# Optimization experiments

Measured on AMD Instinct MI355X. Metric: run time of the kernel, lower is better.

Reference implementation:

```python
import jax, jax.numpy as jnp
import numpy as np

D_MODEL = 1024
N_HEADS = 16
D_HEAD = D_MODEL // N_HEADS
D_FF = 4096
MAX_ITERS = 2
B, T = 8, 1024
LN_EPS = 1e-5


def _layernorm(x, g, b):
    m = jnp.mean(x, axis=-1, keepdims=True)
    v = jnp.mean(jnp.square(x - m), axis=-1, keepdims=True)
    return (x - m) * jax.lax.rsqrt(v + LN_EPS) * g + b


def setup_inputs() -> dict:
    key = jax.random.key(0)
    ks = jax.random.split(key, 16)
    s = 0.02
    inp = {
        "z": jax.random.normal(ks[0], (B, T, D_MODEL), dtype=jnp.float32),
        # per-head Q/K/V projections stacked over heads: [H, D, Dh], bias [H, Dh]
        "Wq": jax.random.normal(ks[1], (N_HEADS, D_MODEL, D_HEAD), dtype=jnp.float32) * s,
        "bq": jnp.zeros((N_HEADS, D_HEAD), dtype=jnp.float32),
        "Wk": jax.random.normal(ks[2], (N_HEADS, D_MODEL, D_HEAD), dtype=jnp.float32) * s,
        "bk": jnp.zeros((N_HEADS, D_HEAD), dtype=jnp.float32),
        "Wv": jax.random.normal(ks[3], (N_HEADS, D_MODEL, D_HEAD), dtype=jnp.float32) * s,
        "bv": jnp.zeros((N_HEADS, D_HEAD), dtype=jnp.float32),
        "Wo": jax.random.normal(ks[4], (D_MODEL, D_MODEL), dtype=jnp.float32) * s,
        "bo": jnp.zeros((D_MODEL,), dtype=jnp.float32),
        "W1": jax.random.normal(ks[5], (D_MODEL, D_FF), dtype=jnp.float32) * s,
        "b1": jnp.zeros((D_FF,), dtype=jnp.float32),
        "W2": jax.random.normal(ks[6], (D_FF, D_MODEL), dtype=jnp.float32) * s,
        "b2": jnp.zeros((D_MODEL,), dtype=jnp.float32),
        "g1": jnp.ones((D_MODEL,), dtype=jnp.float32),
        "be1": jnp.zeros((D_MODEL,), dtype=jnp.float32),
        "g2": jnp.ones((D_MODEL,), dtype=jnp.float32),
        "be2": jnp.zeros((D_MODEL,), dtype=jnp.float32),
    }
    return inp


def reference(z, Wq, bq, Wk, bk, Wv, bv, Wo, bo, W1, b1, W2, b2, g1, be1, g2, be2):
    # Controller outputs (alphas/state/aux) are unused by the original forward -> omitted.
    # Dropout is inference-identity.
    scale = 1.0 / jnp.sqrt(jnp.asarray(D_HEAD, dtype=z.dtype))
    z_refined = z
    for _ in range(MAX_ITERS):
        # batched per-head projections: [B,H,T,Dh]
        q = jnp.einsum('btd,hdk->bhtk', z, Wq) + bq[None, :, None, :]
        k = jnp.einsum('btd,hdk->bhtk', z, Wk) + bk[None, :, None, :]
        v = jnp.einsum('btd,hdk->bhtk', z, Wv) + bv[None, :, None, :]
        scores = jnp.einsum('bhtk,bhsk->bhts', q, k) * scale  # [B,H,T,T]
        attn = jax.nn.softmax(scores, axis=-1)
        o = jnp.einsum('bhts,bhsk->bhtk', attn, v)  # [B,H,T,Dh]
        # concat heads in order (matches torch.cat over head list)
        o = jnp.transpose(o, (0, 2, 1, 3)).reshape(z.shape[0], z.shape[1], D_MODEL)
        attn_out = o @ Wo + bo
        z = _layernorm(z + attn_out, g1, be1)
        z_refined = z
        ffn = jnp.maximum(z @ W1 + b1, 0.0) @ W2 + b2
        z = _layernorm(z + ffn, g2, be2)
    return z_refined
```

## Files before the change

### kernel.cpp

```cpp
#include <hip/hip_runtime.h>
#include <hip/hip_bf16.h>

typedef __bf16 bf16t;
typedef bf16t bf16x4 __attribute__((ext_vector_type(4)));
typedef bf16t bf16x8 __attribute__((ext_vector_type(8)));
typedef float f32x4 __attribute__((ext_vector_type(4)));

#define BT 8192
#define TT 1024
#define DM 1024
#define DFF 4096

static __device__ __forceinline__ f32x4 mfma16(bf16x8 a, bf16x8 b, f32x4 c) {
  return __builtin_amdgcn_mfma_f32_16x16x32_bf16(a, b, c, 0, 0, 0);
}
static __device__ __forceinline__ bf16x8 ld8(const bf16t* p0, const bf16t* p1) {
  bf16x4 lo = *(const bf16x4*)p0;
  bf16x4 hi = *(const bf16x4*)p1;
  return __builtin_shufflevector(lo, hi, 0, 1, 2, 3, 4, 5, 6, 7);
}
static __device__ __forceinline__ f32x4 f4zero() {
  f32x4 z = {0.f, 0.f, 0.f, 0.f};
  return z;
}
static __device__ __forceinline__ f32x4 vmax4(f32x4 a, f32x4 b) {
  f32x4 r;
#pragma unroll
  for (int i = 0; i < 4; i++) r[i] = fmaxf(a[i], b[i]);
  return r;
}
static __device__ __forceinline__ void gld16(const bf16t* g, bf16t* l) {
  __builtin_amdgcn_global_load_lds((const __attribute__((address_space(1))) void*)g,
                                   (__attribute__((address_space(3))) void*)l, 16, 0, 0);
}

__global__ __launch_bounds__(256) void cvt_kernel(const float* __restrict__ in,
                                                  bf16t* __restrict__ out, long n) {
  long i = ((long)blockIdx.x * 256 + threadIdx.x) * 4;
  if (i >= n) return;
  f32x4 v = *(const f32x4*)&in[i];
  bf16x4 o = {(bf16t)v[0], (bf16t)v[1], (bf16t)v[2], (bf16t)v[3]};
  *(bf16x4*)&out[i] = o;
}

__global__ __launch_bounds__(256) void tcvt_kernel(const float* __restrict__ in,
                                                   bf16t* __restrict__ out, int M, int N) {
  __shared__ float T[64][65];
  const int t = threadIdx.x;
  const int ty = t >> 6, tx = t & 63;
  const long n0 = (long)blockIdx.x * 64, m0 = (long)blockIdx.y * 64;
#pragma unroll
  for (int p = 0; p < 16; ++p) {
    int a = ty * 16 + p;
    T[a][tx] = in[(m0 + a) * N + n0 + tx];
  }
  __syncthreads();
#pragma unroll
  for (int p = 0; p < 16; ++p) {
    int r = ty * 16 + p;
    out[(n0 + r) * M + m0 + tx] = (bf16t)T[tx][r];
  }
}

__global__ __launch_bounds__(256) void vtrans_kernel(const bf16t* __restrict__ qkv,
                                                     bf16t* __restrict__ vT) {
  __shared__ bf16t T[64][72];
  const int bh = blockIdx.x;
  const int b = bh >> 4, h = bh & 15;
  const int tt = blockIdx.y;
  const int t = threadIdx.x;
  const int ty = t >> 6, tx = t & 63;
  const long srcbase = ((long)b * TT + tt * 64) * 3072 + 2048 + h * 64;
#pragma unroll
  for (int p = 0; p < 16; ++p) {
    int a = ty * 16 + p;
    T[a][tx] = qkv[srcbase + (long)a * 3072 + tx];
  }
  __syncthreads();
  const long dstbase = ((long)bh * 64) * 1024 + tt * 64;
#pragma unroll
  for (int p = 0; p < 16; ++p) {
    int d = ty * 16 + p;
    vT[dstbase + (long)d * 1024 + tx] = T[tx][d];
  }
}

__global__ __launch_bounds__(256) void pack_qkv_t_kernel(const float* __restrict__ Wq,
                                                         const float* __restrict__ Wk,
                                                         const float* __restrict__ Wv,
                                                         bf16t* __restrict__ WT) {
  __shared__ float T[64][65];
  const int bx = blockIdx.x;
  const int sel = bx >> 4, h = bx & 15;
  const float* src = ((sel == 0) ? Wq : (sel == 1) ? Wk : Wv) + (long)h * 65536;
  const long nbase = (long)sel * 1024 + h * 64;
  const long m0 = (long)blockIdx.y * 64;
  const int t = threadIdx.x;
  const int ty = t >> 6, tx = t & 63;
#pragma unroll
  for (int p = 0; p < 16; ++p) {
    int a = ty * 16 + p;
    T[a][tx] = src[(m0 + a) * 64 + tx];
  }
  __syncthreads();
#pragma unroll
  for (int p = 0; p < 16; ++p) {
    int r = ty * 16 + p;
    WT[(nbase + r) * 1024 + m0 + tx] = (bf16t)T[tx][r];
  }
}

__global__ __launch_bounds__(256) void pack_bias_kernel(const float* __restrict__ bq,
                                                        const float* __restrict__ bk,
                                                        const float* __restrict__ bv,
                                                        float* __restrict__ bqkv) {
  int i = blockIdx.x * 256 + threadIdx.x;
  if (i >= 3072) return;
  int sel = i >> 10, c = i & 1023;
  bqkv[i] = ((sel == 0) ? bq : (sel == 1) ? bk : bv)[c];
}

template <int EPI>
__global__ __launch_bounds__(256) void gemm_kernel(
    const bf16t* __restrict__ A, const bf16t* __restrict__ Bt,
    const float* __restrict__ bias, const float* __restrict__ resid,
    void* __restrict__ Cout, int M, int N, int K) {
  __shared__ bf16t As[3 * 128 * 32];
  __shared__ bf16t Bs[3 * 128 * 32];
  const int tid = threadIdx.x;
  const int lane = tid & 63;
  const int wid = tid >> 6;
  const int wr = wid >> 1, wc = wid & 1;
  const int g = lane >> 4, lr = lane & 15;

  const int gy = M >> 7;
  const int nwg = gridDim.x;
  const int chunk = nwg >> 3;
  const int wg = blockIdx.x;
  const int lid = (wg & 7) * chunk + (wg >> 3);
  const int gsz = gy << 3;
  const int group = lid / gsz;
  const int rem = lid - group * gsz;
  const int rr = rem >> 3;
  const int cc = (group << 3) + (rem & 7);
  const long brow = (long)rr * 128;
  const long bcol = (long)cc * 128;

  f32x4 acc[4][4];
#pragma unroll
  for (int i = 0; i < 4; i++)
#pragma unroll
    for (int j = 0; j < 4; j++) acc[i][j] = f4zero();

  const int srow = tid >> 2;
  const int csrc = (tid & 3) ^ ((tid >> 3) & 3);
  const bf16t* gA = &A[(brow + srow) * (long)K + 8 * csrc];
  const bf16t* gB = &Bt[(bcol + srow) * (long)K + 8 * csrc];
  bf16t* lA = As + wid * 512;
  bf16t* lB = Bs + wid * 512;

  const int xsw = ((lr >> 1) & 3) << 3;
  const int ra0 = (4 * g) ^ xsw;
  const int ra1 = (16 + 4 * g) ^ xsw;

  auto stage = [&](int buf, int k0) {
    gld16(gA + k0, lA + buf * 4096);
    gld16(gA + k0 + (long)64 * K, lA + buf * 4096 + 2048);
    gld16(gB + k0, lB + buf * 4096);
    gld16(gB + k0 + (long)64 * K, lB + buf * 4096 + 2048);
  };

  const int nt = K >> 5;
  stage(0, 0);
  stage(1, 32);
  asm volatile("s_waitcnt vmcnt(4)" ::: "memory");
  __builtin_amdgcn_s_barrier();
  __builtin_amdgcn_sched_barrier(0);

  for (int t = 0; t < nt; ++t) {
    const int k2 = (t + 2) << 5;
    const bool pf = (k2 < K);
    if (pf) stage((t + 2) % 3, k2);

    const bf16t* bufA = As + (t % 3) * 4096;
    const bf16t* bufB = Bs + (t % 3) * 4096;
    bf16x8 af[4], bfv[4];
#pragma unroll
    for (int i = 0; i < 4; i++) {
      const bf16t* r = bufA + (wr * 64 + i * 16 + lr) * 32;
      af[i] = ld8(r + ra0, r + ra1);
    }
#pragma unroll
    for (int j = 0; j < 4; j++) {
      const bf16t* c = bufB + (wc * 64 + j * 16 + lr) * 32;
      bfv[j] = ld8(c + ra0, c + ra1);
    }
#pragma unroll
    for (int i = 0; i < 4; i++)
#pragma unroll
      for (int j = 0; j < 4; j++) acc[i][j] = mfma16(af[i], bfv[j], acc[i][j]);

    if (t + 1 < nt) {
      if (pf)
        asm volatile("s_waitcnt vmcnt(4)" ::: "memory");
      else
        asm volatile("s_waitcnt vmcnt(0)" ::: "memory");
      __builtin_amdgcn_s_barrier();
      __builtin_amdgcn_sched_barrier(0);
    }
  }

#pragma unroll
  for (int j = 0; j < 4; j++) {
    int col = (int)bcol + wc * 64 + j * 16 + lr;
    float bval = bias ? bias[col] : 0.f;
#pragma unroll
    for (int i = 0; i < 4; i++) {
      long row0 = brow + wr * 64 + i * 16 + 4 * g;
#pragma unroll
      for (int r2 = 0; r2 < 4; r2++) {
        long row = row0 + r2;
        float v = acc[i][j][r2] + bval;
        if (EPI == 0) {
          ((bf16t*)Cout)[row * N + col] = (bf16t)v;
        } else if (EPI == 1) {
          ((bf16t*)Cout)[row * N + col] = (bf16t)fmaxf(v, 0.f);
        } else {
          ((float*)Cout)[row * N + col] = v + resid[row * N + col];
        }
      }
    }
  }
}

__global__ __launch_bounds__(256) void attn_kernel(const bf16t* __restrict__ qkv,
                                                   const bf16t* __restrict__ vT,
                                                   bf16t* __restrict__ o) {
  const int bh = blockIdx.x;
  const int b = bh >> 4, h = bh & 15;
  const int qt = blockIdx.y;
  const int tid = threadIdx.x;
  const int lane = tid & 63;
  const int w = tid >> 6;
  const int g = lane >> 4, lr = lane & 15;

  __shared__ bf16t Qs[64 * 64];
  __shared__ bf16t Ks[2][64 * 64];
  __shared__ bf16t Vs[2][64 * 64];

  const long rowbase = (long)b * TT;
  const long qrow0 = rowbase + (long)qt * 64;

  const int srow_in_call = w * 8 + (lane >> 3);
  const int schunk = (lane & 7) ^ ((lane >> 3) & 7);
  const int soff = 8 * schunk;

  const bf16t* qsrc = &qkv[(qrow0 + srow_in_call) * 3072 + h * 64 + soff];
  const bf16t* ksrc = &qkv[(rowbase + srow_in_call) * 3072 + 1024 + h * 64 + soff];
  const bf16t* vsrc = &vT[((long)bh * 64 + srow_in_call) * 1024 + soff];
  bf16t* ldst = (bf16t*)((w * 8) * 64);

  auto stageQ = [&]() {
    gld16(qsrc, Qs + (size_t)ldst);
    gld16(qsrc + (long)32 * 3072, Qs + (size_t)ldst + 32 * 64);
  };
  auto stageK = [&](int buf, int kt) {
    const bf16t* s = ksrc + (long)kt * 64 * 3072;
    gld16(s, Ks[buf] + (size_t)ldst);
    gld16(s + (long)32 * 3072, Ks[buf] + (size_t)ldst + 32 * 64);
  };
  auto stageV = [&](int buf, int kt) {
    const bf16t* s = vsrc + kt * 64;
    gld16(s, Vs[buf] + (size_t)ldst);
    gld16(s + (long)32 * 1024, Vs[buf] + (size_t)ldst + 32 * 64);
  };

  stageQ();
  stageK(0, 0);
  stageV(0, 0);
  __syncthreads();

  const int swk = (lr & 7) << 3;
  const int o0 = (4 * g) ^ swk, o1 = (16 + 4 * g) ^ swk;
  const int o2 = (32 + 4 * g) ^ swk, o3 = (48 + 4 * g) ^ swk;

  const bf16t* qrow = Qs + (w * 16 + lr) * 64;
  const bf16x8 qb_lo = ld8(qrow + o0, qrow + o1);
  const bf16x8 qb_hi = ld8(qrow + o2, qrow + o3);

  f32x4 acc_o[4];
#pragma unroll
  for (int j = 0; j < 4; j++) acc_o[j] = f4zero();
  float mrun = -1e30f, lrun = 0.f;

  int cur = 0;
  for (int kt = 0; kt < 16; ++kt) {
    if (kt < 15) {
      stageK(cur ^ 1, kt + 1);
      stageV(cur ^ 1, kt + 1);
    }

    f32x4 s[4];
#pragma unroll
    for (int jt = 0; jt < 4; jt++) {
      const bf16t* krow = Ks[cur] + (jt * 16 + lr) * 64;
      bf16x8 ka_lo = ld8(krow + o0, krow + o1);
      bf16x8 ka_hi = ld8(krow + o2, krow + o3);
      f32x4 t = f4zero();
      t = mfma16(ka_lo, qb_lo, t);
      t = mfma16(ka_hi, qb_hi, t);
      s[jt] = t;
    }

#pragma unroll
    for (int jt = 0; jt < 4; jt++)
#pragma unroll
      for (int r = 0; r < 4; r++) s[jt][r] *= 0.125f;

    f32x4 mv = vmax4(vmax4(s[0], s[1]), vmax4(s[2], s[3]));
    float tm = fmaxf(fmaxf(mv[0], mv[1]), fmaxf(mv[2], mv[3]));
    tm = fmaxf(tm, __shfl_xor(tm, 16, 64));
    tm = fmaxf(tm, __shfl_xor(tm, 32, 64));

    float mnew = fmaxf(mrun, tm);
    float corr = __expf(mrun - mnew);
    mrun = mnew;

    f32x4 sv = f4zero();
#pragma unroll
    for (int jt = 0; jt < 4; jt++)
#pragma unroll
      for (int r = 0; r < 4; r++) {
        float pv = __expf(s[jt][r] - mnew);
        s[jt][r] = pv;
        sv[r] += pv;
      }
    float tsum = sv[0] + sv[1] + sv[2] + sv[3];
    tsum += __shfl_xor(tsum, 16, 64);
    tsum += __shfl_xor(tsum, 32, 64);
    lrun = lrun * corr + tsum;

#pragma unroll
    for (int r = 0; r < 4; r++) {
      float cq = __shfl(corr, 20 * g + r, 64);
#pragma unroll
      for (int dt = 0; dt < 4; dt++) acc_o[dt][r] *= cq;
    }

    bf16x8 pa0, pa1;
#pragma unroll
    for (int r = 0; r < 4; r++) {
      pa0[r] = (bf16t)s[0][r];
      pa0[r + 4] = (bf16t)s[1][r];
      pa1[r] = (bf16t)s[2][r];
      pa1[r + 4] = (bf16t)s[3][r];
    }

#pragma unroll
    for (int dt = 0; dt < 4; dt++) {
      const bf16t* vrow = Vs[cur] + (dt * 16 + lr) * 64;
      bf16x8 vb_lo = ld8(vrow + o0, vrow + o1);
      bf16x8 vb_hi = ld8(vrow + o2, vrow + o3);
      acc_o[dt] = mfma16(pa0, vb_lo, acc_o[dt]);
      acc_o[dt] = mfma16(pa1, vb_hi, acc_o[dt]);
    }

    __syncthreads();
    cur ^= 1;
  }

  float inv = 1.0f / lrun;
#pragma unroll
  for (int r = 0; r < 4; r++) {
    float iq = __shfl(inv, 20 * g + r, 64);
    long row = qrow0 + w * 16 + 4 * g + r;
#pragma unroll
    for (int dt = 0; dt < 4; dt++) {
      o[row * (long)DM + h * 64 + dt * 16 + lr] = (bf16t)(acc_o[dt][r] * iq);
    }
  }
}

__global__ __launch_bounds__(256) void ln_kernel(const float* __restrict__ x,
                                                 const float* __restrict__ gamma,
                                                 const float* __restrict__ beta,
                                                 bf16t* __restrict__ out_bf,
                                                 float* __restrict__ out_f32) {
  const long row = blockIdx.x;
  const int tid = threadIdx.x;
  const float* xr = x + row * DM;
  f32x4 v = *(const f32x4*)&xr[tid * 4];
  float s = v[0] + v[1] + v[2] + v[3];
  float ss = v[0] * v[0] + v[1] * v[1] + v[2] * v[2] + v[3] * v[3];
#pragma unroll
  for (int m = 1; m < 64; m <<= 1) {
    s += __shfl_xor(s, m, 64);
    ss += __shfl_xor(ss, m, 64);
  }
  __shared__ float red[8];
  const int w = tid >> 6, lane = tid & 63;
  if (lane == 0) {
    red[w] = s;
    red[4 + w] = ss;
  }
  __syncthreads();
  s = red[0] + red[1] + red[2] + red[3];
  ss = red[4] + red[5] + red[6] + red[7];
  float mean = s * (1.f / DM);
  float var = ss * (1.f / DM) - mean * mean;
  float inv = rsqrtf(var + 1e-5f);
  f32x4 ga = *(const f32x4*)&gamma[tid * 4];
  f32x4 be = *(const f32x4*)&beta[tid * 4];
  bf16x4 ob;
  f32x4 of;
#pragma unroll
  for (int c = 0; c < 4; c++) {
    float y = (v[c] - mean) * inv * ga[c] + be[c];
    ob[c] = (bf16t)y;
    of[c] = y;
  }
  long base = row * DM + tid * 4;
  if (out_bf) *(bf16x4*)&out_bf[base] = ob;
  if (out_f32) *(f32x4*)&out_f32[base] = of;
}

extern "C" void kernel_launch(void* const* d_in, const int* in_sizes, int n_in,
                              void* d_out, int out_size, void* d_ws, size_t ws_size,
                              hipStream_t stream) {
  const float* z = (const float*)d_in[0];
  const float* Wq = (const float*)d_in[1];
  const float* bq = (const float*)d_in[2];
  const float* Wk = (const float*)d_in[3];
  const float* bk = (const float*)d_in[4];
  const float* Wv = (const float*)d_in[5];
  const float* bv = (const float*)d_in[6];
  const float* Wo = (const float*)d_in[7];
  const float* bo = (const float*)d_in[8];
  const float* W1 = (const float*)d_in[9];
  const float* b1 = (const float*)d_in[10];
  const float* W2 = (const float*)d_in[11];
  const float* b2 = (const float*)d_in[12];
  const float* g1 = (const float*)d_in[13];
  const float* be1 = (const float*)d_in[14];
  const float* g2 = (const float*)d_in[15];
  const float* be2 = (const float*)d_in[16];

  char* p = (char*)d_ws;
  auto alloc = [&](size_t bytes) {
    char* r = p;
    p += (bytes + 255) & ~(size_t)255;
    return r;
  };
  bf16t* wqkvT = (bf16t*)alloc((size_t)3072 * 1024 * 2);
  float* bqkv = (float*)alloc((size_t)3072 * 4);
  bf16t* woT = (bf16t*)alloc((size_t)1024 * 1024 * 2);
  bf16t* w1T = (bf16t*)alloc((size_t)4096 * 1024 * 2);
  bf16t* w2T = (bf16t*)alloc((size_t)1024 * 4096 * 2);
  bf16t* act = (bf16t*)alloc((size_t)BT * 1024 * 2);
  bf16t* obuf = (bf16t*)alloc((size_t)BT * 1024 * 2);
  bf16t* big = (bf16t*)alloc((size_t)BT * 4096 * 2);
  float* tbuf = (float*)alloc((size_t)BT * 1024 * 4);
  float* residf = (float*)alloc((size_t)BT * 1024 * 4);
  bf16t* vT = (bf16t*)tbuf;

  pack_qkv_t_kernel<<<dim3(48, 16), dim3(256), 0, stream>>>(Wq, Wk, Wv, wqkvT);
  pack_bias_kernel<<<dim3(12), dim3(256), 0, stream>>>(bq, bk, bv, bqkv);
  tcvt_kernel<<<dim3(16, 16), dim3(256), 0, stream>>>(Wo, woT, 1024, 1024);
  tcvt_kernel<<<dim3(64, 16), dim3(256), 0, stream>>>(W1, w1T, 1024, 4096);
  tcvt_kernel<<<dim3(16, 64), dim3(256), 0, stream>>>(W2, w2T, 4096, 1024);
  cvt_kernel<<<dim3(8192), dim3(256), 0, stream>>>(z, act, (long)BT * 1024);

  for (int iter = 0; iter < 2; ++iter) {
    gemm_kernel<0><<<dim3(1536), dim3(256), 0, stream>>>(
        act, wqkvT, bqkv, (const float*)nullptr, (void*)big, BT, 3072, 1024);
    vtrans_kernel<<<dim3(128, 16), dim3(256), 0, stream>>>(big, vT);
    attn_kernel<<<dim3(128, 16), dim3(256), 0, stream>>>(big, vT, obuf);
    const float* rsrc = (iter == 0) ? z : residf;
    gemm_kernel<2><<<dim3(512), dim3(256), 0, stream>>>(
        obuf, woT, bo, rsrc, (void*)tbuf, BT, 1024, 1024);
    if (iter == 1) {
      ln_kernel<<<dim3(8192), dim3(256), 0, stream>>>(tbuf, g1, be1, (bf16t*)nullptr,
                                                      (float*)d_out);
      break;
    }
    ln_kernel<<<dim3(8192), dim3(256), 0, stream>>>(tbuf, g1, be1, act, residf);
    gemm_kernel<1><<<dim3(2048), dim3(256), 0, stream>>>(
        act, w1T, b1, (const float*)nullptr, (void*)big, BT, 4096, 1024);
    gemm_kernel<2><<<dim3(512), dim3(256), 0, stream>>>(
        big, w2T, b2, residf, (void*)tbuf, BT, 1024, 4096);
    ln_kernel<<<dim3(8192), dim3(256), 0, stream>>>(tbuf, g2, be2, act, residf);
  }
}
```

Measured before the change: 697.2 us.

## Add 256x256-tile 512-thread GEMM for QKV and FFN-up projections

Introduces a new GEMM kernel with 256x256 output tiles, 8 waves per block, K-step 64 and double-buffered swizzled LDS. It replaces the 128x128 GEMM for the QKV projection and the first FFN matmul. The larger tiles raise arithmetic intensity and cut global/LDS traffic per FLOP. In exchange each block uses 128KB of LDS and a large accumulator register file, which lowers occupancy. The grid is also much smaller (384/512 blocks on 256 CUs), so tail effects can get worse.

```diff
diff --git a/kernel.cpp b/kernel.cpp
--- a/kernel.cpp
+++ b/kernel.cpp
@@ -118,6 +118,118 @@
   if (i >= 3072) return;
   int sel = i >> 10, c = i & 1023;
   bqkv[i] = ((sel == 0) ? bq : (sel == 1) ? bk : bv)[c];
+}
+
+template <int EPI>
+__global__ __launch_bounds__(512, 2) void gemm256_kernel(
+    const bf16t* __restrict__ A, const bf16t* __restrict__ Bt,
+    const float* __restrict__ bias, const float* __restrict__ resid,
+    void* __restrict__ Cout, int M, int N, int K) {
+  __shared__ bf16t As[2 * 256 * 64];
+  __shared__ bf16t Bs[2 * 256 * 64];
+  const int tid = threadIdx.x;
+  const int lane = tid & 63;
+  const int wid = tid >> 6;
+  const int wm = wid >> 2;
+  const int wn = wid & 3;
+  const int g = lane >> 4, lr = lane & 15;
+
+  const int gy = M >> 8;
+  const int nwg = gridDim.x;
+  const int chunk = nwg >> 3;
+  const int wg = blockIdx.x;
+  const int lid = (wg & 7) * chunk + (wg >> 3);
+  const int gsz = gy << 2;
+  const int group = lid / gsz;
+  const int rem = lid - group * gsz;
+  const int rr = rem >> 2;
+  const int cc = (group << 2) + (rem & 3);
+  const long brow = (long)rr * 256;
+  const long bcol = (long)cc * 256;
+
+  f32x4 acc[8][4];
+#pragma unroll
+  for (int i = 0; i < 8; i++)
+#pragma unroll
+    for (int j = 0; j < 4; j++) acc[i][j] = f4zero();
+
+  const int srow = tid >> 3;
+  const int schunk = (tid & 7) ^ (srow & 7);
+  const bf16t* gA = &A[(brow + srow) * (long)K + 8 * schunk];
+  const bf16t* gB = &Bt[(bcol + srow) * (long)K + 8 * schunk];
+  bf16t* dA0 = As + wid * 512;
+  bf16t* dB0 = Bs + wid * 512;
+
+  auto stage = [&](int buf, int k0) {
+#pragma unroll
+    for (int c = 0; c < 4; ++c) {
+      gld16(gA + k0 + (long)(c * 64) * K, dA0 + buf * 16384 + c * 4096);
+      gld16(gB + k0 + (long)(c * 64) * K, dB0 + buf * 16384 + c * 4096);
+    }
+  };
+
+  const int kr = lr & 7;
+  const int wb = (g & 1) * 4;
+  const int lo0 = (((g >> 1) + 0) ^ kr) * 8 + wb;
+  const int hi0 = (((g >> 1) + 2) ^ kr) * 8 + wb;
+  const int lo1 = (((g >> 1) + 4) ^ kr) * 8 + wb;
+  const int hi1 = (((g >> 1) + 6) ^ kr) * 8 + wb;
+
+  const int nt = K >> 6;
+  stage(0, 0);
+  __syncthreads();
+
+  for (int t = 0; t < nt; ++t) {
+    const int buf = t & 1;
+    if (t + 1 < nt) stage(buf ^ 1, (t + 1) << 6);
+
+    const bf16t* bA = As + buf * 16384;
+    const bf16t* bB = Bs + buf * 16384;
+#pragma unroll
+    for (int s = 0; s < 2; ++s) {
+      const int lo = s ? lo1 : lo0, hi = s ? hi1 : hi0;
+      bf16x8 a[8], b[4];
+#pragma unroll
+      for (int i = 0; i < 8; i++) {
+        const bf16t* r = bA + (wm * 128 + i * 16 + lr) * 64;
+        a[i] = ld8(r + lo, r + hi);
+      }
+#pragma unroll
+      for (int j = 0; j < 4; j++) {
+        const bf16t* c = bB + (wn * 64 + j * 16 + lr) * 64;
+        b[j] = ld8(c + lo, c + hi);
+      }
+      __builtin_amdgcn_s_setprio(1);
+#pragma unroll
+      for (int i = 0; i < 8; i++)
+#pragma unroll
+        for (int j = 0; j < 4; j++) acc[i][j] = mfma16(a[i], b[j], acc[i][j]);
+      __builtin_amdgcn_s_setprio(0);
+    }
+    __syncthreads();
+  }
+
+#pragma unroll
+  for (int j = 0; j < 4; j++) {
+    int col = (int)bcol + wn * 64 + j * 16 + lr;
+    float bval = bias ? bias[col] : 0.f;
+#pragma unroll
+    for (int i = 0; i < 8; i++) {
+      long row0 = brow + wm * 128 + i * 16 + 4 * g;
+#pragma unroll
+      for (int r2 = 0; r2 < 4; r2++) {
+        long row = row0 + r2;
+        float v = acc[i][j][r2] + bval;
+        if (EPI == 0) {
+          ((bf16t*)Cout)[row * N + col] = (bf16t)v;
+        } else if (EPI == 1) {
+          ((bf16t*)Cout)[row * N + col] = (bf16t)fmaxf(v, 0.f);
+        } else {
+          ((float*)Cout)[row * N + col] = v + resid[row * N + col];
+        }
+      }
+    }
+  }
 }
 
 template <int EPI>
@@ -471,7 +583,7 @@
   cvt_kernel<<<dim3(8192), dim3(256), 0, stream>>>(z, act, (long)BT * 1024);
 
   for (int iter = 0; iter < 2; ++iter) {
-    gemm_kernel<0><<<dim3(1536), dim3(256), 0, stream>>>(
+    gemm256_kernel<0><<<dim3(384), dim3(512), 0, stream>>>(
         act, wqkvT, bqkv, (const float*)nullptr, (void*)big, BT, 3072, 1024);
     vtrans_kernel<<<dim3(128, 16), dim3(256), 0, stream>>>(big, vT);
     attn_kernel<<<dim3(128, 16), dim3(256), 0, stream>>>(big, vT, obuf);
@@ -484,7 +596,7 @@
       break;
     }
     ln_kernel<<<dim3(8192), dim3(256), 0, stream>>>(tbuf, g1, be1, act, residf);
-    gemm_kernel<1><<<dim3(2048), dim3(256), 0, stream>>>(
+    gemm256_kernel<1><<<dim3(512), dim3(512), 0, stream>>>(
         act, w1T, b1, (const float*)nullptr, (void*)big, BT, 4096, 1024);
     gemm_kernel<2><<<dim3(512), dim3(256), 0, stream>>>(
         big, w2T, b2, residf, (void*)tbuf, BT, 1024, 4096);
```

Measured after the change: 742.5 us. 6.5% more time.

## Permute K columns for single 16-byte LDS fragment loads; bf16 residual buffers

Applied to the files above, without the earlier changes.

Applies a column permutation (cperm) within each 32-wide K chunk to all GEMM operands (weights, activations, attention output, FFN hidden), so each lane's MFMA fragment is contiguous and loads with one 16-byte LDS read instead of two 8-byte reads. Separately, the residual and pre-LayerNorm buffers move from fp32 to bf16, halving their memory traffic in the GEMM epilogues and LN kernels. The permuted layouts must stay consistent across every producer and consumer, and bf16 residuals reduce accuracy.

```diff
diff --git a/kernel.cpp b/kernel.cpp
--- a/kernel.cpp
+++ b/kernel.cpp
@@ -33,14 +33,21 @@
   __builtin_amdgcn_global_load_lds((const __attribute__((address_space(1))) void*)g,
                                    (__attribute__((address_space(3))) void*)l, 16, 0, 0);
 }
-
-__global__ __launch_bounds__(256) void cvt_kernel(const float* __restrict__ in,
-                                                  bf16t* __restrict__ out, long n) {
+static __device__ __forceinline__ int cperm(int c) {
+  return (c & ~31) + (((c >> 2) & 3) << 3) + (((c >> 4) & 1) << 2) + (c & 3);
+}
+
+__global__ __launch_bounds__(256) void cvtz_kernel(const float* __restrict__ in,
+                                                   bf16t* __restrict__ outp,
+                                                   bf16t* __restrict__ outn, long n) {
   long i = ((long)blockIdx.x * 256 + threadIdx.x) * 4;
   if (i >= n) return;
   f32x4 v = *(const f32x4*)&in[i];
   bf16x4 o = {(bf16t)v[0], (bf16t)v[1], (bf16t)v[2], (bf16t)v[3]};
-  *(bf16x4*)&out[i] = o;
+  *(bf16x4*)&outn[i] = o;
+  int lo = (int)(i & 1023);
+  long p = (i - lo) + cperm(lo);
+  *(bf16x4*)&outp[p] = o;
 }
 
 __global__ __launch_bounds__(256) void tcvt_kernel(const float* __restrict__ in,
@@ -58,7 +65,7 @@
 #pragma unroll
   for (int p = 0; p < 16; ++p) {
     int r = ty * 16 + p;
-    out[(n0 + r) * M + m0 + tx] = (bf16t)T[tx][r];
+    out[(n0 + r) * M + m0 + cperm(tx)] = (bf16t)T[tx][r];
   }
 }
 
@@ -106,7 +113,7 @@
 #pragma unroll
   for (int p = 0; p < 16; ++p) {
     int r = ty * 16 + p;
-    WT[(nbase + r) * 1024 + m0 + tx] = (bf16t)T[tx][r];
+    WT[(nbase + r) * 1024 + m0 + cperm(tx)] = (bf16t)T[tx][r];
   }
 }
 
@@ -123,10 +130,10 @@
 template <int EPI>
 __global__ __launch_bounds__(256) void gemm_kernel(
     const bf16t* __restrict__ A, const bf16t* __restrict__ Bt,
-    const float* __restrict__ bias, const float* __restrict__ resid,
+    const float* __restrict__ bias, const bf16t* __restrict__ resid,
     void* __restrict__ Cout, int M, int N, int K) {
-  __shared__ bf16t As[3 * 128 * 32];
-  __shared__ bf16t Bs[3 * 128 * 32];
+  __shared__ __align__(16) bf16t As[3 * 128 * 32];
+  __shared__ __align__(16) bf16t Bs[3 * 128 * 32];
   const int tid = threadIdx.x;
   const int lane = tid & 63;
   const int wid = tid >> 6;
@@ -159,16 +166,15 @@
   bf16t* lA = As + wid * 512;
   bf16t* lB = Bs + wid * 512;
 
-  const int xsw = ((lr >> 1) & 3) << 3;
-  const int ra0 = (4 * g) ^ xsw;
-  const int ra1 = (16 + 4 * g) ^ xsw;
-
   auto stage = [&](int buf, int k0) {
     gld16(gA + k0, lA + buf * 4096);
     gld16(gA + k0 + (long)64 * K, lA + buf * 4096 + 2048);
     gld16(gB + k0, lB + buf * 4096);
     gld16(gB + k0 + (long)64 * K, lB + buf * 4096 + 2048);
   };
+  auto ldf = [&](const bf16t* buf, int row) -> bf16x8 {
+    return *(const bf16x8*)(buf + row * 32 + ((((row >> 1) ^ g) & 3) << 3));
+  };
 
   const int nt = K >> 5;
   stage(0, 0);
@@ -186,15 +192,9 @@
     const bf16t* bufB = Bs + (t % 3) * 4096;
     bf16x8 af[4], bfv[4];
 #pragma unroll
-    for (int i = 0; i < 4; i++) {
-      const bf16t* r = bufA + (wr * 64 + i * 16 + lr) * 32;
-      af[i] = ld8(r + ra0, r + ra1);
-    }
-#pragma unroll
-    for (int j = 0; j < 4; j++) {
-      const bf16t* c = bufB + (wc * 64 + j * 16 + lr) * 32;
-      bfv[j] = ld8(c + ra0, c + ra1);
-    }
+    for (int i = 0; i < 4; i++) af[i] = ldf(bufA, wr * 64 + i * 16 + lr);
+#pragma unroll
+    for (int j = 0; j < 4; j++) bfv[j] = ldf(bufB, wc * 64 + j * 16 + lr);
 #pragma unroll
     for (int i = 0; i < 4; i++)
 #pragma unroll
@@ -224,9 +224,9 @@
         if (EPI == 0) {
           ((bf16t*)Cout)[row * N + col] = (bf16t)v;
         } else if (EPI == 1) {
-          ((bf16t*)Cout)[row * N + col] = (bf16t)fmaxf(v, 0.f);
+          ((bf16t*)Cout)[row * N + cperm(col)] = (bf16t)fmaxf(v, 0.f);
         } else {
-          ((float*)Cout)[row * N + col] = v + resid[row * N + col];
+          ((bf16t*)Cout)[row * N + col] = (bf16t)(v + (float)resid[row * N + col]);
         }
       }
     }
@@ -244,9 +244,9 @@
   const int w = tid >> 6;
   const int g = lane >> 4, lr = lane & 15;
 
-  __shared__ bf16t Qs[64 * 64];
-  __shared__ bf16t Ks[2][64 * 64];
-  __shared__ bf16t Vs[2][64 * 64];
+  __shared__ __align__(16) bf16t Qs[64 * 64];
+  __shared__ __align__(16) bf16t Ks[2][64 * 64];
+  __shared__ __align__(16) bf16t Vs[2][64 * 64];
 
   const long rowbase = (long)b * TT;
   const long qrow0 = rowbase + (long)qt * 64;
@@ -376,20 +376,24 @@
     long row = qrow0 + w * 16 + 4 * g + r;
 #pragma unroll
     for (int dt = 0; dt < 4; dt++) {
-      o[row * (long)DM + h * 64 + dt * 16 + lr] = (bf16t)(acc_o[dt][r] * iq);
-    }
-  }
-}
-
-__global__ __launch_bounds__(256) void ln_kernel(const float* __restrict__ x,
+      o[row * (long)DM + cperm(h * 64 + dt * 16 + lr)] = (bf16t)(acc_o[dt][r] * iq);
+    }
+  }
+}
+
+__global__ __launch_bounds__(256) void ln_kernel(const bf16t* __restrict__ x,
                                                  const float* __restrict__ gamma,
                                                  const float* __restrict__ beta,
-                                                 bf16t* __restrict__ out_bf,
+                                                 bf16t* __restrict__ out_act,
+                                                 bf16t* __restrict__ out_res,
                                                  float* __restrict__ out_f32) {
   const long row = blockIdx.x;
   const int tid = threadIdx.x;
-  const float* xr = x + row * DM;
-  f32x4 v = *(const f32x4*)&xr[tid * 4];
+  const int idx = tid * 4;
+  bf16x4 xv = *(const bf16x4*)&x[row * DM + idx];
+  float v[4];
+#pragma unroll
+  for (int c = 0; c < 4; c++) v[c] = (float)xv[c];
   float s = v[0] + v[1] + v[2] + v[3];
   float ss = v[0] * v[0] + v[1] * v[1] + v[2] * v[2] + v[3] * v[3];
 #pragma unroll
@@ -409,19 +413,23 @@
   float mean = s * (1.f / DM);
   float var = ss * (1.f / DM) - mean * mean;
   float inv = rsqrtf(var + 1e-5f);
-  f32x4 ga = *(const f32x4*)&gamma[tid * 4];
-  f32x4 be = *(const f32x4*)&beta[tid * 4];
-  bf16x4 ob;
-  f32x4 of;
-#pragma unroll
-  for (int c = 0; c < 4; c++) {
-    float y = (v[c] - mean) * inv * ga[c] + be[c];
-    ob[c] = (bf16t)y;
-    of[c] = y;
-  }
-  long base = row * DM + tid * 4;
-  if (out_bf) *(bf16x4*)&out_bf[base] = ob;
-  if (out_f32) *(f32x4*)&out_f32[base] = of;
+  f32x4 ga = *(const f32x4*)&gamma[idx];
+  f32x4 be = *(const f32x4*)&beta[idx];
+  float y[4];
+#pragma unroll
+  for (int c = 0; c < 4; c++) y[c] = (v[c] - mean) * inv * ga[c] + be[c];
+  if (out_act) {
+    bf16x4 ob = {(bf16t)y[0], (bf16t)y[1], (bf16t)y[2], (bf16t)y[3]};
+    *(bf16x4*)&out_act[row * DM + cperm(idx)] = ob;
+  }
+  if (out_res) {
+    bf16x4 ob = {(bf16t)y[0], (bf16t)y[1], (bf16t)y[2], (bf16t)y[3]};
+    *(bf16x4*)&out_res[row * DM + idx] = ob;
+  }
+  if (out_f32) {
+    f32x4 of = {y[0], y[1], y[2], y[3]};
+    *(f32x4*)&out_f32[row * DM + idx] = of;
+  }
 }
 
 extern "C" void kernel_launch(void* const* d_in, const int* in_sizes, int n_in,
@@ -457,10 +465,11 @@
   bf16t* w1T = (bf16t*)alloc((size_t)4096 * 1024 * 2);
   bf16t* w2T = (bf16t*)alloc((size_t)1024 * 4096 * 2);
   bf16t* act = (bf16t*)alloc((size_t)BT * 1024 * 2);
+  bf16t* zbf = (bf16t*)alloc((size_t)BT * 1024 * 2);
   bf16t* obuf = (bf16t*)alloc((size_t)BT * 1024 * 2);
   bf16t* big = (bf16t*)alloc((size_t)BT * 4096 * 2);
-  float* tbuf = (float*)alloc((size_t)BT * 1024 * 4);
-  float* residf = (float*)alloc((size_t)BT * 1024 * 4);
+  bf16t* tbuf = (bf16t*)alloc((size_t)BT * 1024 * 2);
+  bf16t* residf = (bf16t*)alloc((size_t)BT * 1024 * 2);
   bf16t* vT = (bf16t*)tbuf;
 
   pack_qkv_t_kernel<<<dim3(48, 16), dim3(256), 0, stream>>>(Wq, Wk, Wv, wqkvT);
@@ -468,26 +477,28 @@
   tcvt_kernel<<<dim3(16, 16), dim3(256), 0, stream>>>(Wo, woT, 1024, 1024);
   tcvt_kernel<<<dim3(64, 16), dim3(256), 0, stream>>>(W1, w1T, 1024, 4096);
   tcvt_kernel<<<dim3(16, 64), dim3(256), 0, stream>>>(W2, w2T, 4096, 1024);
-  cvt_kernel<<<dim3(8192), dim3(256), 0, stream>>>(z, act, (long)BT * 1024);
+  cvtz_kernel<<<dim3(8192), dim3(256), 0, stream>>>(z, act, zbf, (long)BT * 1024);
 
   for (int iter = 0; iter < 2; ++iter) {
     gemm_kernel<0><<<dim3(1536), dim3(256), 0, stream>>>(
-        act, wqkvT, bqkv, (const float*)nullptr, (void*)big, BT, 3072, 1024);
+        act, wqkvT, bqkv, (const bf16t*)nullptr, (void*)big, BT, 3072, 1024);
     vtrans_kernel<<<dim3(128, 16), dim3(256), 0, stream>>>(big, vT);
     attn_kernel<<<dim3(128, 16), dim3(256), 0, stream>>>(big, vT, obuf);
-    const float* rsrc = (iter == 0) ? z : residf;
+    const bf16t* rsrc = (iter == 0) ? zbf : residf;
     gemm_kernel<2><<<dim3(512), dim3(256), 0, stream>>>(
         obuf, woT, bo, rsrc, (void*)tbuf, BT, 1024, 1024);
     if (iter == 1) {
       ln_kernel<<<dim3(8192), dim3(256), 0, stream>>>(tbuf, g1, be1, (bf16t*)nullptr,
-                                                      (float*)d_out);
+                                                      (bf16t*)nullptr, (float*)d_out);
       break;
     }
-    ln_kernel<<<dim3(8192), dim3(256), 0, stream>>>(tbuf, g1, be1, act, residf);
+    ln_kernel<<<dim3(8192), dim3(256), 0, stream>>>(tbuf, g1, be1, act, residf,
+                                                    (float*)nullptr);
     gemm_kernel<1><<<dim3(2048), dim3(256), 0, stream>>>(
-        act, w1T, b1, (const float*)nullptr, (void*)big, BT, 4096, 1024);
+        act, w1T, b1, (const bf16t*)nullptr, (void*)big, BT, 4096, 1024);
     gemm_kernel<2><<<dim3(512), dim3(256), 0, stream>>>(
         big, w2T, b2, residf, (void*)tbuf, BT, 1024, 4096);
-    ln_kernel<<<dim3(8192), dim3(256), 0, stream>>>(tbuf, g2, be2, act, residf);
-  }
-}
+    ln_kernel<<<dim3(8192), dim3(256), 0, stream>>>(tbuf, g2, be2, act, residf,
+                                                    (float*)nullptr);
+  }
+}
```

New measurement: 622.9 us. 10.7% less time.
